# Kernel tuning notes

Measured on AMD Instinct MI355X. Metric: run time of the kernel, lower is better.

The kernel has to match this reference:

```python
import jax, jax.numpy as jnp
import numpy as np

N, IN_C, OUT_C = 4096, 256, 64
ALPHA = 0.2  # LeakyReLU negative slope


def setup_inputs() -> dict:
    key = jax.random.key(0)
    k1, k2, k3, k4 = jax.random.split(key, 4)
    H = jax.random.normal(k1, (N, IN_C), dtype=jnp.float32)
    adj = jax.random.randint(k2, (N, N), 0, 2, dtype=jnp.int32)
    # xavier_uniform with gain=1.414
    gain = 1.414
    limW = gain * np.sqrt(6.0 / (IN_C + OUT_C))
    W = jax.random.uniform(k3, (IN_C, OUT_C), minval=-limW, maxval=limW, dtype=jnp.float32)
    lima = gain * np.sqrt(6.0 / (2 * OUT_C + 1))
    a = jax.random.uniform(k4, (2 * OUT_C, 1), minval=-lima, maxval=lima, dtype=jnp.float32)
    return {"H": H, "adj": adj, "W": W, "a": a}


def reference(H, adj, W, a):
    Wh = H @ W  # [N, out_C]
    # Attention_Mat[i,j] = concat(Wh_i, Wh_j); score = Attention_Mat @ a
    # = (Wh @ a1)_i + (Wh @ a2)_j  -- fused, avoids the O(N^2 * 2F) tensor.
    a1, a2 = a[:OUT_C, 0], a[OUT_C:, 0]
    e = (Wh @ a1)[:, None] + (Wh @ a2)[None, :]  # [N, N]
    e = jnp.where(e > 0, e, ALPHA * e)  # LeakyReLU
    att = jax.nn.softmax(e, axis=1)
    # NOTE: original masks AFTER softmax (rows are not renormalized).
    att = jnp.where(adj > 0, att, jnp.zeros_like(att))
    out = att @ Wh  # [N, out_C]
    return jax.nn.elu(out)  # concat=True
```

## Files before the change

### kernel.cpp

```cpp
#include <hip/hip_runtime.h>
#include <math.h>

static constexpr int NN   = 4096;
static constexpr int INC  = 256;
static constexpr int OUTC = 64;

typedef _Float16 half8 __attribute__((ext_vector_type(8)));
typedef float floatx4 __attribute__((ext_vector_type(4)));

__device__ __forceinline__ float lrelu(float x) {
    return fmaxf(x, 0.f) + 0.2f * fminf(x, 0.f);
}
__device__ __forceinline__ float elu1(float x) {
    return x > 0.f ? x : (__expf(x) - 1.f);
}

__global__ __launch_bounds__(256) void k_wh(const float* __restrict__ H,
                                            const float* __restrict__ W,
                                            const float* __restrict__ a,
                                            unsigned short* __restrict__ WhT,
                                            float* __restrict__ f1,
                                            float* __restrict__ f2) {
    __shared__ __align__(16) float Wl[INC * OUTC];
    __shared__ __align__(16) float Hl[16 * INC];
    __shared__ _Float16 Tl[16 * 68];
    const int t = threadIdx.x;
    const int i0 = blockIdx.x * 16;
    {
        const float4* W4 = (const float4*)W;
        float4* Wl4 = (float4*)Wl;
        #pragma unroll
        for (int u = 0; u < 16; ++u) Wl4[u * 256 + t] = W4[u * 256 + t];
        const float4* H4 = (const float4*)(H + i0 * INC);
        float4* Hl4 = (float4*)Hl;
        #pragma unroll
        for (int u = 0; u < 4; ++u) Hl4[u * 256 + t] = H4[u * 256 + t];
    }
    __syncthreads();
    const int c = t & 63;
    const int g = t >> 6;
    const float a1c = a[c];
    const float a2c = a[OUTC + c];
    float acc[4] = {0.f, 0.f, 0.f, 0.f};
    const float4* Hl4 = (const float4*)Hl;
    for (int k4 = 0; k4 < INC / 4; ++k4) {
        const float w0 = Wl[(k4 * 4 + 0) * OUTC + c];
        const float w1 = Wl[(k4 * 4 + 1) * OUTC + c];
        const float w2 = Wl[(k4 * 4 + 2) * OUTC + c];
        const float w3 = Wl[(k4 * 4 + 3) * OUTC + c];
        #pragma unroll
        for (int s = 0; s < 4; ++s) {
            const float4 h = Hl4[(g + 4 * s) * (INC / 4) + k4];
            acc[s] = fmaf(h.x, w0, fmaf(h.y, w1, fmaf(h.z, w2, fmaf(h.w, w3, acc[s]))));
        }
    }
    #pragma unroll
    for (int s = 0; s < 4; ++s) {
        const int r = g + 4 * s;
        Tl[r * 68 + c] = (_Float16)acc[s];
        float v1 = acc[s] * a1c;
        float v2 = acc[s] * a2c;
        #pragma unroll
        for (int off = 32; off; off >>= 1) {
            v1 += __shfl_xor(v1, off);
            v2 += __shfl_xor(v2, off);
        }
        if (c == 0) { f1[i0 + r] = v1; f2[i0 + r] = v2; }
    }
    __syncthreads();
    const int c2 = t >> 2;
    const int rs = (t & 3) * 4;
    ushort4 u;
    u.x = *(const unsigned short*)&Tl[(rs + 0) * 68 + c2];
    u.y = *(const unsigned short*)&Tl[(rs + 1) * 68 + c2];
    u.z = *(const unsigned short*)&Tl[(rs + 2) * 68 + c2];
    u.w = *(const unsigned short*)&Tl[(rs + 3) * 68 + c2];
    *(ushort4*)(WhT + c2 * NN + i0 + rs) = u;
}

__global__ __launch_bounds__(1024, 4) void k_att(const int* __restrict__ adj,
                                                 const _Float16* __restrict__ WhT,
                                                 const float* __restrict__ f1,
                                                 const float* __restrict__ f2,
                                                 float* __restrict__ out) {
    __shared__ __align__(16) float sf2[NN];
    __shared__ __align__(16) float sacc[16 * 1024];
    __shared__ float sden[16 * 16];
    __shared__ float smax[16];
    const int t = threadIdx.x;
    const int w = t >> 6;
    const int l = t & 63;
    const int m = l & 15;
    const int quad = l >> 4;
    const int i0 = blockIdx.x * 16;

    {
        const float4 v = ((const float4*)f2)[t];
        ((float4*)sf2)[t] = v;
        float mloc = fmaxf(fmaxf(v.x, v.y), fmaxf(v.z, v.w));
        #pragma unroll
        for (int off = 32; off; off >>= 1) mloc = fmaxf(mloc, __shfl_xor(mloc, off));
        if (l == 0) smax[w] = mloc;
    }
    __syncthreads();
    float maxf2 = smax[0];
    #pragma unroll
    for (int k = 1; k < 16; ++k) maxf2 = fmaxf(maxf2, smax[k]);

    const float f1r = f1[i0 + m];
    const float mrow = lrelu(f1r + maxf2);
    float den = 0.f;
    floatx4 acc[4] = {{0.f,0.f,0.f,0.f},{0.f,0.f,0.f,0.f},{0.f,0.f,0.f,0.f},{0.f,0.f,0.f,0.f}};
    const int jbase = w * 32 + quad * 8;
    const int* adjrow = adj + (size_t)(i0 + m) * NN;

    #pragma unroll 2
    for (int it = 0; it < 8; ++it) {
        const int j = jbase + it * 512;
        const int4 a0 = *(const int4*)(adjrow + j);
        const int4 a1 = *(const int4*)(adjrow + j + 4);
        const float4 g0 = *(const float4*)(sf2 + j);
        const float4 g1 = *(const float4*)(sf2 + j + 4);
        half8 af;
        {
            float p;
            p = __expf(lrelu(f1r + g0.x) - mrow); den += p; af[0] = (a0.x > 0) ? (_Float16)p : (_Float16)0.f;
            p = __expf(lrelu(f1r + g0.y) - mrow); den += p; af[1] = (a0.y > 0) ? (_Float16)p : (_Float16)0.f;
            p = __expf(lrelu(f1r + g0.z) - mrow); den += p; af[2] = (a0.z > 0) ? (_Float16)p : (_Float16)0.f;
            p = __expf(lrelu(f1r + g0.w) - mrow); den += p; af[3] = (a0.w > 0) ? (_Float16)p : (_Float16)0.f;
            p = __expf(lrelu(f1r + g1.x) - mrow); den += p; af[4] = (a1.x > 0) ? (_Float16)p : (_Float16)0.f;
            p = __expf(lrelu(f1r + g1.y) - mrow); den += p; af[5] = (a1.y > 0) ? (_Float16)p : (_Float16)0.f;
            p = __expf(lrelu(f1r + g1.z) - mrow); den += p; af[6] = (a1.z > 0) ? (_Float16)p : (_Float16)0.f;
            p = __expf(lrelu(f1r + g1.w) - mrow); den += p; af[7] = (a1.w > 0) ? (_Float16)p : (_Float16)0.f;
        }
        #pragma unroll
        for (int nt = 0; nt < 4; ++nt) {
            const half8 bf = *(const half8*)(WhT + (size_t)(nt * 16 + m) * NN + j);
            acc[nt] = __builtin_amdgcn_mfma_f32_16x16x32_f16(af, bf, acc[nt], 0, 0, 0);
        }
    }
    den += __shfl_xor(den, 16);
    den += __shfl_xor(den, 32);
    if (l < 16) sden[w * 16 + l] = den;
    #pragma unroll
    for (int nt = 0; nt < 4; ++nt)
        #pragma unroll
        for (int r = 0; r < 4; ++r)
            sacc[w * 1024 + (quad * 4 + r) * 64 + nt * 16 + m] = acc[nt][r];
    __syncthreads();
    float s = 0.f;
    #pragma unroll
    for (int w2 = 0; w2 < 16; ++w2) s += sacc[w2 * 1024 + t];
    float dden = 0.f;
    const int row = t >> 6;
    #pragma unroll
    for (int w2 = 0; w2 < 16; ++w2) dden += sden[w2 * 16 + row];
    out[(size_t)i0 * OUTC + t] = elu1(s / dden);
}

extern "C" void kernel_launch(void* const* d_in, const int* in_sizes, int n_in,
                              void* d_out, int out_size, void* d_ws, size_t ws_size,
                              hipStream_t stream) {
    const float* H  = (const float*)d_in[0];
    const int* adj  = (const int*)d_in[1];
    const float* W  = (const float*)d_in[2];
    const float* a  = (const float*)d_in[3];
    float* out = (float*)d_out;
    char* ws = (char*)d_ws;
    unsigned short* WhT = (unsigned short*)(ws);
    float* f1   = (float*)(ws + (512 << 10));
    float* f2   = (float*)(ws + (528 << 10));
    hipLaunchKernelGGL(k_wh,  dim3(256), dim3(256),  0, stream, H, W, a, WhT, f1, f2);
    hipLaunchKernelGGL(k_att, dim3(256), dim3(1024), 0, stream, adj, (const _Float16*)WhT, f1, f2, out);
}
```

Measured before the change: 128.5 us.

## Pack adjacency into a bitmask in a pre-pass before the attention kernel

Adds a k_pack kernel that turns the int32 adjacency matrix into a 1-bit-per-entry mask in workspace. The attention kernel then loads eight mask bytes per thread up front instead of streaming two int4 adjacency vectors per iteration. The aim is to take the large, latency-heavy adj loads out of the MFMA/exp inner loop. The full 64MB of adjacency is still read each call, now by a separate kernel, so this adds a launch and a small extra write and read of the bitmask.

```diff
diff --git a/kernel.cpp b/kernel.cpp
--- a/kernel.cpp
+++ b/kernel.cpp
@@ -13,6 +13,23 @@
 }
 __device__ __forceinline__ float elu1(float x) {
     return x > 0.f ? x : (__expf(x) - 1.f);
+}
+
+__global__ __launch_bounds__(256) void k_pack(const int* __restrict__ adj,
+                                              unsigned int* __restrict__ bits) {
+    const int tau = blockIdx.x * 256 + threadIdx.x;
+    const int4* src = (const int4*)adj + (size_t)tau * 8;
+    unsigned int out = 0;
+    #pragma unroll
+    for (int u = 0; u < 8; ++u) {
+        const int4 v = src[u];
+        const unsigned int nib = (unsigned int)(v.x > 0)
+                               | ((unsigned int)(v.y > 0) << 1)
+                               | ((unsigned int)(v.z > 0) << 2)
+                               | ((unsigned int)(v.w > 0) << 3);
+        out |= nib << (4 * u);
+    }
+    bits[tau] = out;
 }
 
 __global__ __launch_bounds__(256) void k_wh(const float* __restrict__ H,
@@ -78,7 +95,7 @@
     *(ushort4*)(WhT + c2 * NN + i0 + rs) = u;
 }
 
-__global__ __launch_bounds__(1024, 4) void k_att(const int* __restrict__ adj,
+__global__ __launch_bounds__(1024, 4) void k_att(const unsigned char* __restrict__ bits,
                                                  const _Float16* __restrict__ WhT,
                                                  const float* __restrict__ f1,
                                                  const float* __restrict__ f2,
@@ -112,26 +129,28 @@
     float den = 0.f;
     floatx4 acc[4] = {{0.f,0.f,0.f,0.f},{0.f,0.f,0.f,0.f},{0.f,0.f,0.f,0.f},{0.f,0.f,0.f,0.f}};
     const int jbase = w * 32 + quad * 8;
-    const int* adjrow = adj + (size_t)(i0 + m) * NN;
+    const unsigned char* brow = bits + (size_t)(i0 + m) * (NN / 8) + (jbase >> 3);
+    unsigned int m8[8];
+    #pragma unroll
+    for (int it = 0; it < 8; ++it) m8[it] = brow[it * 64];
 
     #pragma unroll 2
     for (int it = 0; it < 8; ++it) {
         const int j = jbase + it * 512;
-        const int4 a0 = *(const int4*)(adjrow + j);
-        const int4 a1 = *(const int4*)(adjrow + j + 4);
+        const unsigned int mb = m8[it];
         const float4 g0 = *(const float4*)(sf2 + j);
         const float4 g1 = *(const float4*)(sf2 + j + 4);
         half8 af;
         {
             float p;
-            p = __expf(lrelu(f1r + g0.x) - mrow); den += p; af[0] = (a0.x > 0) ? (_Float16)p : (_Float16)0.f;
-            p = __expf(lrelu(f1r + g0.y) - mrow); den += p; af[1] = (a0.y > 0) ? (_Float16)p : (_Float16)0.f;
-            p = __expf(lrelu(f1r + g0.z) - mrow); den += p; af[2] = (a0.z > 0) ? (_Float16)p : (_Float16)0.f;
-            p = __expf(lrelu(f1r + g0.w) - mrow); den += p; af[3] = (a0.w > 0) ? (_Float16)p : (_Float16)0.f;
-            p = __expf(lrelu(f1r + g1.x) - mrow); den += p; af[4] = (a1.x > 0) ? (_Float16)p : (_Float16)0.f;
-            p = __expf(lrelu(f1r + g1.y) - mrow); den += p; af[5] = (a1.y > 0) ? (_Float16)p : (_Float16)0.f;
-            p = __expf(lrelu(f1r + g1.z) - mrow); den += p; af[6] = (a1.z > 0) ? (_Float16)p : (_Float16)0.f;
-            p = __expf(lrelu(f1r + g1.w) - mrow); den += p; af[7] = (a1.w > 0) ? (_Float16)p : (_Float16)0.f;
+            p = __expf(lrelu(f1r + g0.x) - mrow); den += p; af[0] = (mb & 1u)   ? (_Float16)p : (_Float16)0.f;
+            p = __expf(lrelu(f1r + g0.y) - mrow); den += p; af[1] = (mb & 2u)   ? (_Float16)p : (_Float16)0.f;
+            p = __expf(lrelu(f1r + g0.z) - mrow); den += p; af[2] = (mb & 4u)   ? (_Float16)p : (_Float16)0.f;
+            p = __expf(lrelu(f1r + g0.w) - mrow); den += p; af[3] = (mb & 8u)   ? (_Float16)p : (_Float16)0.f;
+            p = __expf(lrelu(f1r + g1.x) - mrow); den += p; af[4] = (mb & 16u)  ? (_Float16)p : (_Float16)0.f;
+            p = __expf(lrelu(f1r + g1.y) - mrow); den += p; af[5] = (mb & 32u)  ? (_Float16)p : (_Float16)0.f;
+            p = __expf(lrelu(f1r + g1.z) - mrow); den += p; af[6] = (mb & 64u)  ? (_Float16)p : (_Float16)0.f;
+            p = __expf(lrelu(f1r + g1.w) - mrow); den += p; af[7] = (mb & 128u) ? (_Float16)p : (_Float16)0.f;
         }
         #pragma unroll
         for (int nt = 0; nt < 4; ++nt) {
@@ -168,8 +187,11 @@
     float* out = (float*)d_out;
     char* ws = (char*)d_ws;
     unsigned short* WhT = (unsigned short*)(ws);
-    float* f1   = (float*)(ws + (512 << 10));
-    float* f2   = (float*)(ws + (528 << 10));
-    hipLaunchKernelGGL(k_wh,  dim3(256), dim3(256),  0, stream, H, W, a, WhT, f1, f2);
-    hipLaunchKernelGGL(k_att, dim3(256), dim3(1024), 0, stream, adj, (const _Float16*)WhT, f1, f2, out);
+    float* f1 = (float*)(ws + (512 << 10));
+    float* f2 = (float*)(ws + (528 << 10));
+    unsigned int* bits = (unsigned int*)(ws + (1 << 20));
+    hipLaunchKernelGGL(k_pack, dim3(2048), dim3(256), 0, stream, adj, bits);
+    hipLaunchKernelGGL(k_wh,   dim3(256),  dim3(256), 0, stream, H, W, a, WhT, f1, f2);
+    hipLaunchKernelGGL(k_att,  dim3(256),  dim3(1024), 0, stream,
+                       (const unsigned char*)bits, (const _Float16*)WhT, f1, f2, out);
 }
```

Result: no change. 129.2 us (+0.6%).
